# Kernel tuning notes

Hardware: AMD Instinct MI355X
Metric: run time of the kernel (lower is better)

The kernel has to match this reference:

```python
import jax, jax.numpy as jnp
import numpy as np
import math

EMBED = 1024
HEADS = 16
HEAD_DIM = EMBED // HEADS
B, S = 2, 2048


def setup_inputs() -> dict:
    key = jax.random.key(0)
    ks = jax.random.split(key, 11)
    s = 1.0 / math.sqrt(EMBED)
    return {
        "query": jax.random.normal(ks[0], (B, S, EMBED), jnp.float32),
        "key_": jax.random.normal(ks[1], (B, S, EMBED), jnp.float32),
        "value": jax.random.normal(ks[2], (B, S, EMBED), jnp.float32),
        "Wq": jax.random.normal(ks[3], (EMBED, EMBED), jnp.float32) * s,
        "bq": jax.random.normal(ks[4], (EMBED,), jnp.float32) * s,
        "Wk": jax.random.normal(ks[5], (EMBED, EMBED), jnp.float32) * s,
        "bk": jax.random.normal(ks[6], (EMBED,), jnp.float32) * s,
        "Wv": jax.random.normal(ks[7], (EMBED, EMBED), jnp.float32) * s,
        "bv": jax.random.normal(ks[8], (EMBED,), jnp.float32) * s,
        "Wo": jax.random.normal(ks[9], (EMBED, EMBED), jnp.float32) * s,
        "bo": jax.random.normal(ks[10], (EMBED,), jnp.float32) * s,
    }


def reference(query, key_, value, Wq, bq, Wk, bk, Wv, bv, Wo, bo):
    b, s, e = query.shape
    # projections (torch Linear: x @ W.T + b)
    q = query @ Wq.T + bq
    k = key_ @ Wk.T + bk
    v = value @ Wv.T + bv
    # [B, H, S, hd]
    q = q.reshape(b, s, HEADS, HEAD_DIM).transpose(0, 2, 1, 3)
    k = k.reshape(b, s, HEADS, HEAD_DIM).transpose(0, 2, 1, 3)
    v = v.reshape(b, s, HEADS, HEAD_DIM).transpose(0, 2, 1, 3)
    scores = jnp.einsum("bhqd,bhkd->bhqk", q, k) / math.sqrt(HEAD_DIM)
    attn = jax.nn.softmax(scores, axis=-1)
    out = jnp.einsum("bhqk,bhkd->bhqd", attn, v)
    out = out.transpose(0, 2, 1, 3).reshape(b, s, e)
    return out @ Wo.T + bo
```

## Files before the change

kernel.cpp:

```cpp
#include <hip/hip_runtime.h>
#include <hip/hip_bf16.h>

using bf16_t = __bf16;
using bf16x2 = __attribute__((ext_vector_type(2))) __bf16;
using bf16x4 = __attribute__((ext_vector_type(4))) __bf16;
using bf16x8 = __attribute__((ext_vector_type(8))) __bf16;
using f32x4  = __attribute__((ext_vector_type(4))) float;
using u32 = unsigned int;
using u32x4 = __attribute__((ext_vector_type(4))) u32;
using i32x2 = __attribute__((ext_vector_type(2))) int;

constexpr int S_ = 2048, E_ = 1024, M_ = 4096;
constexpr size_t MAT_A = (size_t)M_ * E_;
constexpr size_t MAT_W = (size_t)E_ * E_;

__device__ __forceinline__ bf16_t tobf(float f) {
  unsigned u = __builtin_bit_cast(unsigned, f);
  unsigned short r = (unsigned short)((u + 0x7fffu + ((u >> 16) & 1u)) >> 16);
  return __builtin_bit_cast(bf16_t, r);
}
__device__ __forceinline__ u32 packbf2(float a, float b) {
  u32 ua = __builtin_bit_cast(u32, a) + 0x8000u;
  u32 ub = __builtin_bit_cast(u32, b) + 0x8000u;
  return (ua >> 16) | (ub & 0xffff0000u);
}
__device__ __forceinline__ u32 cvtpk(float lo, float hi) {
  bf16x2 t;
  t[0] = (bf16_t)lo;
  t[1] = (bf16_t)hi;
  return __builtin_bit_cast(u32, t);
}
__device__ __forceinline__ void swap32(u32& a, u32& b) {
  i32x2 r = __builtin_amdgcn_permlane32_swap((int)a, (int)b, false, false);
  a = (u32)r[0];
  b = (u32)r[1];
}
__device__ __forceinline__ void swap16(u32& a, u32& b) {
  i32x2 r = __builtin_amdgcn_permlane16_swap((int)a, (int)b, false, false);
  a = (u32)r[0];
  b = (u32)r[1];
}
__device__ __forceinline__ void async_lds16(const bf16_t* g, bf16_t* l) {
  __builtin_amdgcn_global_load_lds(
      (const __attribute__((address_space(1))) unsigned int*)g,
      (__attribute__((address_space(3))) unsigned int*)l, 16, 0, 0);
}

__global__ __launch_bounds__(256) void cvt_all(
    const float* __restrict__ s0, const float* __restrict__ s1,
    const float* __restrict__ s2, const float* __restrict__ s3,
    const float* __restrict__ s4, const float* __restrict__ s5,
    const float* __restrict__ s6,
    bf16_t* __restrict__ d0, bf16_t* __restrict__ d1,
    bf16_t* __restrict__ d2, bf16_t* __restrict__ d3,
    bf16_t* __restrict__ d4, bf16_t* __restrict__ d5,
    bf16_t* __restrict__ d6) {
  size_t i8 = ((size_t)blockIdx.x * 256 + threadIdx.x) * 8;
  const float* s;
  bf16_t* d;
  size_t off;
  if (i8 < 3 * MAT_A) {
    int w = (int)(i8 >> 22);
    off = i8 & (MAT_A - 1);
    s = w == 0 ? s0 : w == 1 ? s1 : s2;
    d = w == 0 ? d0 : w == 1 ? d1 : d2;
  } else {
    size_t j = i8 - 3 * MAT_A;
    int w = (int)(j >> 20);
    off = j & (MAT_W - 1);
    s = w == 0 ? s3 : w == 1 ? s4 : w == 2 ? s5 : s6;
    d = w == 0 ? d3 : w == 1 ? d4 : w == 2 ? d5 : d6;
  }
  float4 a = *(const float4*)(s + off);
  float4 b = *(const float4*)(s + off + 4);
  bf16x8 o;
  o[0] = tobf(a.x); o[1] = tobf(a.y); o[2] = tobf(a.z); o[3] = tobf(a.w);
  o[4] = tobf(b.x); o[5] = tobf(b.y); o[6] = tobf(b.z); o[7] = tobf(b.w);
  *(bf16x8*)(d + off) = o;
}

__global__ __launch_bounds__(256) void gemm_qkv(
    const bf16_t* __restrict__ xq, const bf16_t* __restrict__ xk,
    const bf16_t* __restrict__ xv, const bf16_t* __restrict__ wq,
    const bf16_t* __restrict__ wk, const bf16_t* __restrict__ wv,
    const float* __restrict__ bq, const float* __restrict__ bk,
    const float* __restrict__ bv, bf16_t* __restrict__ outb,
    bf16_t* __restrict__ Vt) {
  constexpr int K = 1024, N = 1024, BK = 64;
  constexpr float SC = 0.18033688011f;
  __shared__ __align__(16) bf16_t smem[2][16384];

  const int which = blockIdx.y >> 3;
  const bf16_t* X = which == 0 ? xq : which == 1 ? xk : xv;
  const bf16_t* W = which == 0 ? wq : which == 1 ? wk : wv;
  const float* bias = which == 0 ? bq : which == 1 ? bk : bv;
  const int row0 = blockIdx.x * 128, col0 = (blockIdx.y & 7) * 128;

  const int tid = threadIdx.x, lane = tid & 63, wave = tid >> 6;
  const int l15 = lane & 15, q = lane >> 4;
  const int wm = (wave & 1) * 64, wn = (wave >> 1) * 64;
  const f32x4 fzero = {0.f, 0.f, 0.f, 0.f};

  f32x4 acc[4][4];
#pragma unroll
  for (int i = 0; i < 4; ++i)
#pragma unroll
    for (int j = 0; j < 4; ++j) acc[i][j] = fzero;

  const int srow = lane >> 3;
  const int schunk = ((lane & 7) ^ srow) * 8;
  const bf16_t* gA = X + (size_t)(row0 + wave * 32 + srow) * K + schunk;
  const bf16_t* gB = W + (size_t)(col0 + wave * 32 + srow) * K + schunk;
  const int lofs = wave * 32 * BK;

  int ck[2];
  ck[0] = ((q) ^ (l15 & 7)) * 8;
  ck[1] = ((4 + q) ^ (l15 & 7)) * 8;

#pragma unroll
  for (int p = 0; p < 4; ++p) {
    async_lds16(gA + (size_t)(p * 8) * K, smem[0] + lofs + p * 8 * BK);
    async_lds16(gB + (size_t)(p * 8) * K, smem[0] + 8192 + lofs + p * 8 * BK);
  }

  for (int it = 0; it < 16; ++it) {
    const int cur = it & 1;
    __syncthreads();
    if (it + 1 < 16) {
      const int k1 = (it + 1) * BK;
      bf16_t* dA = smem[cur ^ 1] + lofs;
      bf16_t* dB = smem[cur ^ 1] + 8192 + lofs;
#pragma unroll
      for (int p = 0; p < 4; ++p) {
        async_lds16(gA + k1 + (size_t)(p * 8) * K, dA + p * 8 * BK);
        async_lds16(gB + k1 + (size_t)(p * 8) * K, dB + p * 8 * BK);
      }
    }
    const bf16_t* As = smem[cur];
    const bf16_t* Bs = smem[cur] + 8192;
#pragma unroll
    for (int h = 0; h < 2; ++h) {
      bf16x8 af[4], bw[4];
#pragma unroll
      for (int i = 0; i < 4; ++i)
        af[i] = *(const bf16x8*)(As + (wm + i * 16 + l15) * BK + ck[h]);
#pragma unroll
      for (int j = 0; j < 4; ++j)
        bw[j] = *(const bf16x8*)(Bs + (wn + j * 16 + l15) * BK + ck[h]);
#pragma unroll
      for (int i = 0; i < 4; ++i)
#pragma unroll
        for (int j = 0; j < 4; ++j)
          acc[i][j] = __builtin_amdgcn_mfma_f32_16x16x32_bf16(af[i], bw[j],
                                                              acc[i][j], 0, 0, 0);
    }
  }

  if (which < 2) {
    const float sc = which == 0 ? SC : 1.0f;
    bf16_t* C = outb + (size_t)which * MAT_A;
#pragma unroll
    for (int j = 0; j < 4; ++j) {
      const int col = col0 + wn + j * 16 + l15;
      const float bc = bias[col];
#pragma unroll
      for (int i = 0; i < 4; ++i)
#pragma unroll
        for (int r = 0; r < 4; ++r) {
          const int row = row0 + wm + i * 16 + q * 4 + r;
          C[(size_t)row * N + col] = tobf((acc[i][j][r] + bc) * sc);
        }
    }
  } else {
    __syncthreads();
    bf16_t* Ep = &smem[0][0] + wave * 4608;
#pragma unroll
    for (int j = 0; j < 4; ++j) {
      const float bc = bias[col0 + wn + j * 16 + l15];
      const int nl = j * 16 + l15;
#pragma unroll
      for (int i = 0; i < 4; ++i) {
        uint2 pk;
        pk.x = packbf2(acc[i][j][0] + bc, acc[i][j][1] + bc);
        pk.y = packbf2(acc[i][j][2] + bc, acc[i][j][3] + bc);
        *(uint2*)(Ep + nl * 72 + i * 16 + q * 4) = pk;
      }
    }
    const int head = (col0 + wn) >> 6;
    const int tok0 = row0 + wm;
    const int bb = tok0 >> 11, tokb = tok0 & 2047;
    const int dl = lane >> 3, ml = (lane & 7) * 8;
#pragma unroll
    for (int p = 0; p < 8; ++p) {
      const int d = dl + p * 8;
      bf16x8 v = *(const bf16x8*)(Ep + d * 72 + ml);
      *(bf16x8*)(Vt + ((size_t)((bb * 16 + head) * 64 + d)) * S_ + tokb + ml) = v;
    }
  }
}

__global__ __launch_bounds__(256) void gemm_o(const bf16_t* __restrict__ X,
                                              const bf16_t* __restrict__ W,
                                              const float* __restrict__ bias,
                                              float* __restrict__ C) {
  constexpr int K = 1024, N = 1024, BK = 64;
  __shared__ __align__(16) bf16_t smem[2][12288];
  const int tid = threadIdx.x, lane = tid & 63, wave = tid >> 6;
  const int l15 = lane & 15, q = lane >> 4;
  const int row0 = blockIdx.x * 64, col0 = blockIdx.y * 128;
  const int wm = (wave & 1) * 32, wn = (wave >> 1) * 64;
  const f32x4 fzero = {0.f, 0.f, 0.f, 0.f};

  f32x4 acc[2][4];
#pragma unroll
  for (int i = 0; i < 2; ++i)
#pragma unroll
    for (int j = 0; j < 4; ++j) acc[i][j] = fzero;

  const int srow = lane >> 3;
  const int schunk = ((lane & 7) ^ srow) * 8;
  const bf16_t* gA = X + (size_t)(row0 + wave * 16 + srow) * K + schunk;
  const bf16_t* gB = W + (size_t)(col0 + wave * 32 + srow) * K + schunk;
  const int lofsA = wave * 16 * BK;
  const int lofsB = wave * 32 * BK;

  int ck[2];
  ck[0] = ((q) ^ (l15 & 7)) * 8;
  ck[1] = ((4 + q) ^ (l15 & 7)) * 8;

  async_lds16(gA, smem[0] + lofsA);
  async_lds16(gA + (size_t)8 * K, smem[0] + lofsA + 8 * BK);
#pragma unroll
  for (int p = 0; p < 4; ++p)
    async_lds16(gB + (size_t)(p * 8) * K, smem[0] + 4096 + lofsB + p * 8 * BK);

  for (int it = 0; it < 16; ++it) {
    const int cur = it & 1;
    __syncthreads();
    if (it + 1 < 16) {
      const int k1 = (it + 1) * BK;
      bf16_t* dA = smem[cur ^ 1] + lofsA;
      bf16_t* dB = smem[cur ^ 1] + 4096 + lofsB;
      async_lds16(gA + k1, dA);
      async_lds16(gA + k1 + (size_t)8 * K, dA + 8 * BK);
#pragma unroll
      for (int p = 0; p < 4; ++p)
        async_lds16(gB + k1 + (size_t)(p * 8) * K, dB + p * 8 * BK);
    }
    const bf16_t* As = smem[cur];
    const bf16_t* Bs = smem[cur] + 4096;
#pragma unroll
    for (int h = 0; h < 2; ++h) {
      bf16x8 af[2], bw[4];
#pragma unroll
      for (int i = 0; i < 2; ++i)
        af[i] = *(const bf16x8*)(As + (wm + i * 16 + l15) * BK + ck[h]);
#pragma unroll
      for (int j = 0; j < 4; ++j)
        bw[j] = *(const bf16x8*)(Bs + (wn + j * 16 + l15) * BK + ck[h]);
#pragma unroll
      for (int i = 0; i < 2; ++i)
#pragma unroll
        for (int j = 0; j < 4; ++j)
          acc[i][j] = __builtin_amdgcn_mfma_f32_16x16x32_bf16(af[i], bw[j],
                                                              acc[i][j], 0, 0, 0);
    }
  }

#pragma unroll
  for (int j = 0; j < 4; ++j) {
    const int col = col0 + wn + j * 16 + l15;
    const float bc = bias[col];
#pragma unroll
    for (int i = 0; i < 2; ++i)
#pragma unroll
      for (int r = 0; r < 4; ++r) {
        const int row = row0 + wm + i * 16 + q * 4 + r;
        C[(size_t)row * N + col] = acc[i][j][r] + bc;
      }
  }
}

__global__ __launch_bounds__(256, 2) void attn_mfma(
    const bf16_t* __restrict__ Qm, const bf16_t* __restrict__ Km,
    const bf16_t* __restrict__ Vtg, bf16_t* __restrict__ Om) {
  __shared__ __align__(16) bf16_t Ks[3][64 * 64];
  __shared__ __align__(16) bf16_t Vs[3][64 * 64];

  const int tid = threadIdx.x, lane = tid & 63, wave = tid >> 6;
  const int l15 = lane & 15, q = lane >> 4;
  const int bh = blockIdx.x & 31, qb = blockIdx.x >> 5;
  const int b = bh >> 4, h = bh & 15;
  const size_t rowbase = (size_t)b * S_;
  const int hcol = h * 64;
  const int q0 = qb * 128 + wave * 32;

  const int srow = lane >> 3;
  const int schunk = (lane & 7) ^ srow;
  const bf16_t* gK = Km + (rowbase + wave * 16 + srow) * E_ + hcol + schunk * 8;
  const bf16_t* gV = Vtg + ((size_t)bh * 64 + wave * 16 + srow) * S_ + schunk * 8;

  bf16x8 qf[2][2];
#pragma unroll
  for (int qt = 0; qt < 2; ++qt) {
    const bf16_t* qp = Qm + (rowbase + q0 + qt * 16 + l15) * E_ + hcol + q * 8;
    qf[qt][0] = *(const bf16x8*)qp;
    qf[qt][1] = *(const bf16x8*)(qp + 32);
  }

  bf16x8 onesv;
#pragma unroll
  for (int j = 0; j < 8; ++j)
    onesv[j] = __builtin_bit_cast(bf16_t, (unsigned short)0x3F80);

  const f32x4 fzero = {0.f, 0.f, 0.f, 0.f};
  f32x4 oacc[2][4];
#pragma unroll
  for (int qt = 0; qt < 2; ++qt)
#pragma unroll
    for (int mt = 0; mt < 4; ++mt) oacc[qt][mt] = fzero;
  f32x4 lsacc[2] = {fzero, fzero};

  const int rbase = l15 * 64;
  int ck[2];
  ck[0] = ((q) ^ (l15 & 7)) * 8;
  ck[1] = ((4 + q) ^ (l15 & 7)) * 8;

  auto STAGE = [&](int tile, int bi) {
    const size_t koff = (size_t)(tile * 64) * E_;
    const int voff = tile * 64;
    bf16_t* dK = Ks[bi] + wave * 1024;
    bf16_t* dV = Vs[bi] + wave * 1024;
    async_lds16(gK + koff, dK);
    async_lds16(gK + koff + (size_t)8 * E_, dK + 512);
    async_lds16(gV + voff, dV);
    async_lds16(gV + voff + (size_t)8 * S_, dV + 512);
  };

  auto COMPUTE = [&](const bf16_t* Kbuf, const bf16_t* Vbuf) {
    u32 uu[2][4][2];
#pragma unroll
    for (int nt = 0; nt < 4; ++nt) {
      bf16x8 a0 = *(const bf16x8*)(Kbuf + nt * 1024 + rbase + ck[0]);
      bf16x8 a1 = *(const bf16x8*)(Kbuf + nt * 1024 + rbase + ck[1]);
#pragma unroll
      for (int qt = 0; qt < 2; ++qt) {
        f32x4 st = fzero;
        st = __builtin_amdgcn_mfma_f32_16x16x32_bf16(a0, qf[qt][0], st, 0, 0, 0);
        st = __builtin_amdgcn_mfma_f32_16x16x32_bf16(a1, qf[qt][1], st, 0, 0, 0);
        uu[qt][nt][0] =
            cvtpk(__builtin_amdgcn_exp2f(st[0]), __builtin_amdgcn_exp2f(st[1]));
        uu[qt][nt][1] =
            cvtpk(__builtin_amdgcn_exp2f(st[2]), __builtin_amdgcn_exp2f(st[3]));
      }
    }
#pragma unroll
    for (int kk = 0; kk < 2; ++kk) {
      bf16x8 bp[2];
#pragma unroll
      for (int qt = 0; qt < 2; ++qt) {
        u32 A = uu[qt][2 * kk][0], Bv = uu[qt][2 * kk][1];
        u32 C = uu[qt][2 * kk + 1][0], D = uu[qt][2 * kk + 1][1];
        swap32(A, C);  swap16(A, C);
        swap32(Bv, D); swap16(Bv, D);
        u32x4 w = {A, Bv, C, D};
        bp[qt] = __builtin_bit_cast(bf16x8, w);
        lsacc[qt] = __builtin_amdgcn_mfma_f32_16x16x32_bf16(onesv, bp[qt],
                                                            lsacc[qt], 0, 0, 0);
      }
      __builtin_amdgcn_s_setprio(1);
#pragma unroll
      for (int mt = 0; mt < 4; ++mt) {
        bf16x8 av = *(const bf16x8*)(Vbuf + mt * 1024 + rbase + ck[kk]);
        oacc[0][mt] = __builtin_amdgcn_mfma_f32_16x16x32_bf16(av, bp[0],
                                                              oacc[0][mt], 0, 0, 0);
        oacc[1][mt] = __builtin_amdgcn_mfma_f32_16x16x32_bf16(av, bp[1],
                                                              oacc[1][mt], 0, 0, 0);
      }
      __builtin_amdgcn_s_setprio(0);
    }
  };

  STAGE(0, 0);
  STAGE(1, 1);

  int cur = 0;
  for (int t = 0; t < 31; ++t) {
    asm volatile("s_waitcnt vmcnt(4)" ::: "memory");
    __builtin_amdgcn_sched_barrier(0);
    __builtin_amdgcn_s_barrier();
    if (t + 2 < 32) {
      int nb = cur + 2;
      if (nb >= 3) nb -= 3;
      STAGE(t + 2, nb);
    }
    COMPUTE(Ks[cur], Vs[cur]);
    cur = cur == 2 ? 0 : cur + 1;
  }
  asm volatile("s_waitcnt vmcnt(0)" ::: "memory");
  __builtin_amdgcn_sched_barrier(0);
  __builtin_amdgcn_s_barrier();
  COMPUTE(Ks[cur], Vs[cur]);

#pragma unroll
  for (int qt = 0; qt < 2; ++qt) {
    const float inv = 1.0f / lsacc[qt][0];
    const size_t orow = (rowbase + q0 + qt * 16 + l15) * E_ + hcol + q * 4;
#pragma unroll
    for (int mt = 0; mt < 4; ++mt) {
      bf16x4 o;
#pragma unroll
      for (int r = 0; r < 4; ++r) o[r] = tobf(oacc[qt][mt][r] * inv);
      *(bf16x4*)(Om + orow + mt * 16) = o;
    }
  }
}

extern "C" void kernel_launch(void* const* d_in, const int* in_sizes, int n_in,
                              void* d_out, int out_size, void* d_ws, size_t ws_size,
                              hipStream_t stream) {
  const float* query = (const float*)d_in[0];
  const float* key_  = (const float*)d_in[1];
  const float* value = (const float*)d_in[2];
  const float* Wq = (const float*)d_in[3];
  const float* bq = (const float*)d_in[4];
  const float* Wk = (const float*)d_in[5];
  const float* bk = (const float*)d_in[6];
  const float* Wv = (const float*)d_in[7];
  const float* bv = (const float*)d_in[8];
  const float* Wo = (const float*)d_in[9];
  const float* bo = (const float*)d_in[10];

  bf16_t* qc  = (bf16_t*)d_ws;
  bf16_t* kc  = qc + MAT_A;
  bf16_t* vc  = kc + MAT_A;
  bf16_t* wqb = vc + MAT_A;
  bf16_t* wkb = wqb + MAT_W;
  bf16_t* wvb = wkb + MAT_W;
  bf16_t* wob = wvb + MAT_W;
  bf16_t* Qb  = wob + MAT_W;
  bf16_t* Kb  = Qb + MAT_A;
  bf16_t* Vt  = Kb + MAT_A;
  bf16_t* AOb = Vt + MAT_A;

  cvt_all<<<8192, 256, 0, stream>>>(query, key_, value, Wq, Wk, Wv, Wo,
                                    qc, kc, vc, wqb, wkb, wvb, wob);
  gemm_qkv<<<dim3(32, 24), 256, 0, stream>>>(qc, kc, vc, wqb, wkb, wvb,
                                             bq, bk, bv, Qb, Vt);
  attn_mfma<<<512, 256, 0, stream>>>(Qb, Kb, Vt, AOb);
  gemm_o<<<dim3(64, 8), 256, 0, stream>>>(AOb, wob, bo, (float*)d_out);
}
```

Before: 208.1 us.

## Software-pipeline attention loop: overlap QK of tile t+1 with PV of tile t

Splits the per-tile compute into separate QK (scores+exp) and PV (probability times V) stages. It interleaves the QK of the next K tile with the PV of the previous tile, using double-buffered score registers. The goal is to hide exp/convert latency and dependency stalls between the MFMA chains. LDS buffering grows from 3 to 4 stages so a V tile stays resident one iteration longer, which raises LDS use to 64KB per block and keeps two score register sets live, so occupancy may drop.

New measurement: 210.2 us. About the same (+1.0%).

```diff
diff --git a/kernel.cpp b/kernel.cpp
--- a/kernel.cpp
+++ b/kernel.cpp
@@ -284,8 +284,8 @@
 __global__ __launch_bounds__(256, 2) void attn_mfma(
     const bf16_t* __restrict__ Qm, const bf16_t* __restrict__ Km,
     const bf16_t* __restrict__ Vtg, bf16_t* __restrict__ Om) {
-  __shared__ __align__(16) bf16_t Ks[3][64 * 64];
-  __shared__ __align__(16) bf16_t Vs[3][64 * 64];
+  __shared__ __align__(16) bf16_t Ks[4][64 * 64];
+  __shared__ __align__(16) bf16_t Vs[4][64 * 64];
 
   const int tid = threadIdx.x, lane = tid & 63, wave = tid >> 6;
   const int l15 = lane & 15, q = lane >> 4;
@@ -337,10 +337,9 @@
     async_lds16(gV + voff + (size_t)8 * S_, dV + 512);
   };
 
-  auto COMPUTE = [&](const bf16_t* Kbuf, const bf16_t* Vbuf) {
-    u32 uu[2][4][2];
-#pragma unroll
-    for (int nt = 0; nt < 4; ++nt) {
+  auto QK = [&](const bf16_t* Kbuf, u32 (&uu)[2][4][2], int nt0, int nt1) {
+#pragma unroll
+    for (int nt = nt0; nt < nt1; ++nt) {
       bf16x8 a0 = *(const bf16x8*)(Kbuf + nt * 1024 + rbase + ck[0]);
       bf16x8 a1 = *(const bf16x8*)(Kbuf + nt * 1024 + rbase + ck[1]);
 #pragma unroll
@@ -354,53 +353,85 @@
             cvtpk(__builtin_amdgcn_exp2f(st[2]), __builtin_amdgcn_exp2f(st[3]));
       }
     }
-#pragma unroll
-    for (int kk = 0; kk < 2; ++kk) {
-      bf16x8 bp[2];
-#pragma unroll
-      for (int qt = 0; qt < 2; ++qt) {
-        u32 A = uu[qt][2 * kk][0], Bv = uu[qt][2 * kk][1];
-        u32 C = uu[qt][2 * kk + 1][0], D = uu[qt][2 * kk + 1][1];
-        swap32(A, C);  swap16(A, C);
-        swap32(Bv, D); swap16(Bv, D);
-        u32x4 w = {A, Bv, C, D};
-        bp[qt] = __builtin_bit_cast(bf16x8, w);
-        lsacc[qt] = __builtin_amdgcn_mfma_f32_16x16x32_bf16(onesv, bp[qt],
-                                                            lsacc[qt], 0, 0, 0);
-      }
-      __builtin_amdgcn_s_setprio(1);
-#pragma unroll
-      for (int mt = 0; mt < 4; ++mt) {
-        bf16x8 av = *(const bf16x8*)(Vbuf + mt * 1024 + rbase + ck[kk]);
-        oacc[0][mt] = __builtin_amdgcn_mfma_f32_16x16x32_bf16(av, bp[0],
-                                                              oacc[0][mt], 0, 0, 0);
-        oacc[1][mt] = __builtin_amdgcn_mfma_f32_16x16x32_bf16(av, bp[1],
-                                                              oacc[1][mt], 0, 0, 0);
-      }
-      __builtin_amdgcn_s_setprio(0);
-    }
   };
+
+  auto PV = [&](const bf16_t* Vbuf, u32 (&uu)[2][4][2], int kk) {
+    bf16x8 bp[2];
+#pragma unroll
+    for (int qt = 0; qt < 2; ++qt) {
+      u32 A = uu[qt][2 * kk][0], Bv = uu[qt][2 * kk][1];
+      u32 C = uu[qt][2 * kk + 1][0], D = uu[qt][2 * kk + 1][1];
+      swap32(A, C);  swap16(A, C);
+      swap32(Bv, D); swap16(Bv, D);
+      u32x4 w = {A, Bv, C, D};
+      bp[qt] = __builtin_bit_cast(bf16x8, w);
+      lsacc[qt] = __builtin_amdgcn_mfma_f32_16x16x32_bf16(onesv, bp[qt],
+                                                          lsacc[qt], 0, 0, 0);
+    }
+    __builtin_amdgcn_s_setprio(1);
+#pragma unroll
+    for (int mt = 0; mt < 4; ++mt) {
+      bf16x8 av = *(const bf16x8*)(Vbuf + mt * 1024 + rbase + ck[kk]);
+      oacc[0][mt] = __builtin_amdgcn_mfma_f32_16x16x32_bf16(av, bp[0],
+                                                            oacc[0][mt], 0, 0, 0);
+      oacc[1][mt] = __builtin_amdgcn_mfma_f32_16x16x32_bf16(av, bp[1],
+                                                            oacc[1][mt], 0, 0, 0);
+    }
+    __builtin_amdgcn_s_setprio(0);
+  };
+
+  u32 uuA[2][4][2], uuB[2][4][2];
 
   STAGE(0, 0);
   STAGE(1, 1);
 
-  int cur = 0;
-  for (int t = 0; t < 31; ++t) {
+  asm volatile("s_waitcnt vmcnt(4)" ::: "memory");
+  __builtin_amdgcn_sched_barrier(0);
+  __builtin_amdgcn_s_barrier();
+  STAGE(2, 2);
+  QK(Ks[0], uuA, 0, 4);
+
+#pragma unroll 1
+  for (int t = 1; t < 31; t += 2) {
     asm volatile("s_waitcnt vmcnt(4)" ::: "memory");
     __builtin_amdgcn_sched_barrier(0);
     __builtin_amdgcn_s_barrier();
-    if (t + 2 < 32) {
-      int nb = cur + 2;
-      if (nb >= 3) nb -= 3;
-      STAGE(t + 2, nb);
-    }
-    COMPUTE(Ks[cur], Vs[cur]);
-    cur = cur == 2 ? 0 : cur + 1;
-  }
+    if (t + 2 < 32) STAGE(t + 2, (t + 2) & 3);
+    {
+      const bf16_t* Kb = Ks[t & 3];
+      const bf16_t* Vb = Vs[(t - 1) & 3];
+      QK(Kb, uuB, 0, 2);
+      PV(Vb, uuA, 0);
+      QK(Kb, uuB, 2, 4);
+      PV(Vb, uuA, 1);
+    }
+    asm volatile("s_waitcnt vmcnt(4)" ::: "memory");
+    __builtin_amdgcn_sched_barrier(0);
+    __builtin_amdgcn_s_barrier();
+    if (t + 3 < 32) STAGE(t + 3, (t + 3) & 3);
+    {
+      const bf16_t* Kb = Ks[(t + 1) & 3];
+      const bf16_t* Vb = Vs[t & 3];
+      QK(Kb, uuA, 0, 2);
+      PV(Vb, uuB, 0);
+      QK(Kb, uuA, 2, 4);
+      PV(Vb, uuB, 1);
+    }
+  }
+
   asm volatile("s_waitcnt vmcnt(0)" ::: "memory");
   __builtin_amdgcn_sched_barrier(0);
   __builtin_amdgcn_s_barrier();
-  COMPUTE(Ks[cur], Vs[cur]);
+  {
+    const bf16_t* Kb = Ks[31 & 3];
+    const bf16_t* Vb = Vs[30 & 3];
+    QK(Kb, uuB, 0, 2);
+    PV(Vb, uuA, 0);
+    QK(Kb, uuB, 2, 4);
+    PV(Vb, uuA, 1);
+  }
+  PV(Vs[31 & 3], uuB, 0);
+  PV(Vs[31 & 3], uuB, 1);
 
 #pragma unroll
   for (int qt = 0; qt < 2; ++qt) {
```

## Split KV tiles across two wave groups per attention block and merge partials

Applied to the files above, without the earlier changes.

The attention kernel now runs 512 threads per block as two groups of four waves. Each group handles alternating K/V tiles for the same 128 query rows, using its own double-buffered LDS region. At the end the partial output accumulators and row sums are reduced through LDS before normalising and writing. This aims to double the waves available per query tile so memory latency hides better. In exchange the triple-buffer pipeline becomes a double buffer with a full-block barrier per tile, and the tighter launch bounds add register pressure and a risk of spills.

Result: faster. 202.2 us, median of 2 (-2.8%).

```diff
diff --git a/kernel.cpp b/kernel.cpp
--- a/kernel.cpp
+++ b/kernel.cpp
@@ -281,24 +281,25 @@
   }
 }
 
-__global__ __launch_bounds__(256, 2) void attn_mfma(
+__global__ __launch_bounds__(512, 4) void attn_mfma(
     const bf16_t* __restrict__ Qm, const bf16_t* __restrict__ Km,
     const bf16_t* __restrict__ Vtg, bf16_t* __restrict__ Om) {
-  __shared__ __align__(16) bf16_t Ks[3][64 * 64];
-  __shared__ __align__(16) bf16_t Vs[3][64 * 64];
+  __shared__ __align__(16) bf16_t Ks[2][2][64 * 64];
+  __shared__ __align__(16) bf16_t Vs[2][2][64 * 64];
 
   const int tid = threadIdx.x, lane = tid & 63, wave = tid >> 6;
+  const int g = wave >> 2, wv = wave & 3;
   const int l15 = lane & 15, q = lane >> 4;
   const int bh = blockIdx.x & 31, qb = blockIdx.x >> 5;
   const int b = bh >> 4, h = bh & 15;
   const size_t rowbase = (size_t)b * S_;
   const int hcol = h * 64;
-  const int q0 = qb * 128 + wave * 32;
+  const int q0 = qb * 128 + wv * 32;
 
   const int srow = lane >> 3;
   const int schunk = (lane & 7) ^ srow;
-  const bf16_t* gK = Km + (rowbase + wave * 16 + srow) * E_ + hcol + schunk * 8;
-  const bf16_t* gV = Vtg + ((size_t)bh * 64 + wave * 16 + srow) * S_ + schunk * 8;
+  const bf16_t* gK = Km + (rowbase + wv * 16 + srow) * E_ + hcol + schunk * 8;
+  const bf16_t* gV = Vtg + ((size_t)bh * 64 + wv * 16 + srow) * S_ + schunk * 8;
 
   bf16x8 qf[2][2];
 #pragma unroll
@@ -329,8 +330,8 @@
   auto STAGE = [&](int tile, int bi) {
     const size_t koff = (size_t)(tile * 64) * E_;
     const int voff = tile * 64;
-    bf16_t* dK = Ks[bi] + wave * 1024;
-    bf16_t* dV = Vs[bi] + wave * 1024;
+    bf16_t* dK = Ks[g][bi] + wv * 1024;
+    bf16_t* dV = Vs[g][bi] + wv * 1024;
     async_lds16(gK + koff, dK);
     async_lds16(gK + koff + (size_t)8 * E_, dK + 512);
     async_lds16(gV + voff, dV);
@@ -381,37 +382,52 @@
     }
   };
 
-  STAGE(0, 0);
-  STAGE(1, 1);
-
-  int cur = 0;
-  for (int t = 0; t < 31; ++t) {
-    asm volatile("s_waitcnt vmcnt(4)" ::: "memory");
-    __builtin_amdgcn_sched_barrier(0);
-    __builtin_amdgcn_s_barrier();
-    if (t + 2 < 32) {
-      int nb = cur + 2;
-      if (nb >= 3) nb -= 3;
-      STAGE(t + 2, nb);
-    }
-    COMPUTE(Ks[cur], Vs[cur]);
-    cur = cur == 2 ? 0 : cur + 1;
-  }
-  asm volatile("s_waitcnt vmcnt(0)" ::: "memory");
-  __builtin_amdgcn_sched_barrier(0);
-  __builtin_amdgcn_s_barrier();
-  COMPUTE(Ks[cur], Vs[cur]);
-
-#pragma unroll
-  for (int qt = 0; qt < 2; ++qt) {
-    const float inv = 1.0f / lsacc[qt][0];
-    const size_t orow = (rowbase + q0 + qt * 16 + l15) * E_ + hcol + q * 4;
-#pragma unroll
-    for (int mt = 0; mt < 4; ++mt) {
-      bf16x4 o;
-#pragma unroll
-      for (int r = 0; r < 4; ++r) o[r] = tobf(oacc[qt][mt][r] * inv);
-      *(bf16x4*)(Om + orow + mt * 16) = o;
+  STAGE(g, 0);
+  for (int r = 0; r < 16; ++r) {
+    __syncthreads();
+    if (r + 1 < 16) STAGE(2 * (r + 1) + g, (r + 1) & 1);
+    COMPUTE(Ks[g][r & 1], Vs[g][r & 1]);
+  }
+
+  __syncthreads();
+  float* obuf = (float*)(&Ks[0][0][0]);
+  float* lbuf = (float*)(&Vs[0][0][0]);
+  if (g == 1) {
+    float* ow = obuf + wv * 2048;
+#pragma unroll
+    for (int qt = 0; qt < 2; ++qt)
+#pragma unroll
+      for (int mt = 0; mt < 4; ++mt)
+#pragma unroll
+        for (int r4 = 0; r4 < 4; ++r4)
+          ow[(((qt * 4 + mt) * 4) + r4) * 64 + lane] = oacc[qt][mt][r4];
+    lbuf[wv * 128 + lane] = lsacc[0][0];
+    lbuf[wv * 128 + 64 + lane] = lsacc[1][0];
+  }
+  __syncthreads();
+  if (g == 0) {
+    float* ow = obuf + wv * 2048;
+#pragma unroll
+    for (int qt = 0; qt < 2; ++qt)
+#pragma unroll
+      for (int mt = 0; mt < 4; ++mt)
+#pragma unroll
+        for (int r4 = 0; r4 < 4; ++r4)
+          oacc[qt][mt][r4] += ow[(((qt * 4 + mt) * 4) + r4) * 64 + lane];
+    float lsum[2];
+    lsum[0] = lsacc[0][0] + lbuf[wv * 128 + lane];
+    lsum[1] = lsacc[1][0] + lbuf[wv * 128 + 64 + lane];
+#pragma unroll
+    for (int qt = 0; qt < 2; ++qt) {
+      const float inv = 1.0f / lsum[qt];
+      const size_t orow = (rowbase + q0 + qt * 16 + l15) * E_ + hcol + q * 4;
+#pragma unroll
+      for (int mt = 0; mt < 4; ++mt) {
+        bf16x4 o;
+#pragma unroll
+        for (int r = 0; r < 4; ++r) o[r] = tobf(oacc[qt][mt][r] * inv);
+        *(bf16x4*)(Om + orow + mt * 16) = o;
+      }
     }
   }
 }
@@ -447,6 +463,6 @@
                                     qc, kc, vc, wqb, wkb, wvb, wob);
   gemm_qkv<<<dim3(32, 24), 256, 0, stream>>>(qc, kc, vc, wqb, wkb, wvb,
                                              bq, bk, bv, Qb, Vt);
-  attn_mfma<<<512, 256, 0, stream>>>(Qb, Kb, Vt, AOb);
+  attn_mfma<<<512, 512, 0, stream>>>(Qb, Kb, Vt, AOb);
   gemm_o<<<dim3(64, 8), 256, 0, stream>>>(AOb, wob, bo, (float*)d_out);
 }
```
